# Optimization experiments

Hardware: AMD Instinct MI355X
Metric: run time of the kernel (lower is better)

The kernel has to match this reference:

```python
import jax, jax.numpy as jnp
import numpy as np

N = 27          # num_classes (nodes)
C = 512         # in_channels
B = 64          # batch
EPS = 1e-5


def _bn(x, gamma, beta):
    # BatchNorm1d over [b, channels, feat]: normalize over (batch, feat), training mode (batch stats, biased var)
    mean = jnp.mean(x, axis=(0, 2), keepdims=True)
    var = jnp.mean((x - mean) ** 2, axis=(0, 2), keepdims=True)
    return gamma[None, :, None] * (x - mean) * jax.lax.rsqrt(var + EPS) + beta[None, :, None]


def _layer(x, edge, WA, WB, WE, WU, WV, ge, be, gv, bv):
    # x: [b, n, c], edge: [b, n*n, c]; edge index e = i*n + j; end[e,i]=1, start[e,j]=1
    b = x.shape[0]
    res = x
    Vix = x @ WA.T                       # [b, n, c]  (gathered to edges via end)
    Vjx = x @ WB.T                       # [b, n, c]  (gathered to edges via start)
    e_lin = edge @ WE.T                  # [b, n*n, c]
    # einsum('ev,bvc->bec', end, Vix) == broadcast Vix over j; start gathers Vjx over i
    msg = (Vix[:, :, None, :] + Vjx[:, None, :, :]).reshape(b, N * N, C) + e_lin
    edge = edge + jax.nn.relu(_bn(msg, ge, be))
    # attention: sigmoid then softmax over j (dim 2 of [b, n, n, c])
    e = jax.nn.sigmoid(edge).reshape(b, N, N, C)
    e = jax.nn.softmax(e, axis=2).reshape(b, N * N, C)
    Ujx = x @ WV.T                       # [b, n, c], gathered via start -> broadcast over i
    Ujx_e = jnp.broadcast_to(Ujx[:, None, :, :], (b, N, N, C)).reshape(b, N * N, C)
    Uix = x @ WU.T
    # einsum('ve,bec->bvc', end.T, t) == sum over j of t[b, i*n+j]
    agg = (e * Ujx_e).reshape(b, N, N, C).sum(axis=2)
    x = Uix + agg / N
    x = jax.nn.relu(res + _bn(x, gv, bv))
    return x, edge


def setup_inputs() -> dict:
    key = jax.random.key(0)
    ks = jax.random.split(key, 12)
    scale = np.sqrt(2.0 / C)
    w = lambda k: (jax.random.normal(k, (C, C), dtype=jnp.float32) * scale)
    inp = {
        "x": jax.random.normal(ks[0], (B, N, C), dtype=jnp.float32),
        "edge": jax.random.normal(ks[1], (B, N * N, C), dtype=jnp.float32),
        "WU1": w(ks[2]), "WV1": w(ks[3]), "WA1": w(ks[4]), "WB1": w(ks[5]), "WE1": w(ks[6]),
        "WU2": w(ks[7]), "WV2": w(ks[8]), "WA2": w(ks[9]), "WB2": w(ks[10]), "WE2": w(ks[11]),
        "gv1": jnp.ones((N,), jnp.float32), "bv1": jnp.zeros((N,), jnp.float32),
        "ge1": jnp.ones((N * N,), jnp.float32), "be1": jnp.zeros((N * N,), jnp.float32),
        "gv2": jnp.ones((N,), jnp.float32), "bv2": jnp.zeros((N,), jnp.float32),
        "ge2": jnp.ones((N * N,), jnp.float32), "be2": jnp.zeros((N * N,), jnp.float32),
    }
    return inp


def reference(x, edge, WU1, WV1, WA1, WB1, WE1, WU2, WV2, WA2, WB2, WE2,
              gv1, bv1, ge1, be1, gv2, bv2, ge2, be2):
    x, edge = _layer(x, edge, WA1, WB1, WE1, WU1, WV1, ge1, be1, gv1, bv1)
    x, edge = _layer(x, edge, WA2, WB2, WE2, WU2, WV2, ge2, be2, gv2, bv2)
    return x, edge
```

## Files before the change

kernel.cpp:

```cpp
#include <hip/hip_runtime.h>

typedef unsigned short u16;
typedef unsigned int u32;
typedef __bf16 bf16x8 __attribute__((ext_vector_type(8)));
typedef float f32x4 __attribute__((ext_vector_type(4)));

#define DI __device__ __forceinline__

DI u16 f2bf(float f) {
  union { float f; u32 u; } v; v.f = f;
  return (u16)((v.u + 0x7fffu + ((v.u >> 16) & 1u)) >> 16);
}
DI float bf2f(u16 h) {
  union { u32 u; float f; } v; v.u = ((u32)h) << 16;
  return v.f;
}

DI void gload_lds16(const void* g, void* l) {
  __builtin_amdgcn_global_load_lds((const __attribute__((address_space(1))) u32*)g,
                                   (__attribute__((address_space(3))) u32*)l, 16, 0, 0);
}

constexpr float INV_M = 1.0f / 32768.0f;

__global__ void convw_k(const float* wa1, const float* wb1, const float* wu1, const float* wv1, const float* we1,
                        const float* wa2, const float* wb2, const float* wu2, const float* wv2, const float* we2,
                        u16* dst) {
  int idx = blockIdx.x * 256 + threadIdx.x;
  int m = idx >> 16;
  int i = (idx & 0xffff) << 2;
  const float* s;
  switch (m) {
    case 0: s = wa1; break; case 1: s = wb1; break; case 2: s = wu1; break;
    case 3: s = wv1; break; case 4: s = we1; break; case 5: s = wa2; break;
    case 6: s = wb2; break; case 7: s = wu2; break; case 8: s = wv2; break;
    default: s = we2; break;
  }
  float4 v = *(const float4*)(s + i);
  ushort4 o;
  o.x = f2bf(v.x); o.y = f2bf(v.y); o.z = f2bf(v.z); o.w = f2bf(v.w);
  *(ushort4*)(dst + ((size_t)m << 18) + i) = o;
}

template<int EPI, int ABF>
__global__ __launch_bounds__(256, 5) void gemm_k(
    const void* __restrict__ A_, const u16* __restrict__ W,
    float* __restrict__ outf, int ldout,
    u16* __restrict__ msg, const float* __restrict__ V4,
    float* __restrict__ esum, float* __restrict__ esq) {
  __shared__ __align__(16) u16 lA[64 * 64];
  __shared__ __align__(16) u16 lW[128 * 64];
  const int tid = threadIdx.x;
  const int lane = tid & 63, wid = tid >> 6;
  const int wm = wid >> 1, wn = wid & 1;
  const int q = lane >> 4, l15 = lane & 15;
  const int rb = blockIdx.y, cb = blockIdx.x;
  const int lrow8 = lane >> 3, lg = lane & 7;

  f32x4 acc[2][4];
#pragma unroll
  for (int a = 0; a < 2; a++)
#pragma unroll
    for (int b = 0; b < 4; b++) acc[a][b] = (f32x4){0.f, 0.f, 0.f, 0.f};

  for (int k0 = 0; k0 < 512; k0 += 64) {
    __syncthreads();
    if (ABF) {
#pragma unroll
      for (int it = 0; it < 2; it++) {
        int ch = wid * 2 + it;
        int row = ch * 8 + lrow8;
        const u16* src = (const u16*)A_ + (((size_t)(rb * 64 + row)) << 9) + k0 + ((lg ^ (row & 7)) << 3);
        gload_lds16(src, lA + ch * 512);
      }
    } else {
#pragma unroll
      for (int s = tid; s < 512; s += 256) {
        int row = s >> 3, g = s & 7;
        const float* src = (const float*)A_ + (((size_t)(rb * 64 + row)) << 9) + k0 + g * 8;
        float4 s0 = *(const float4*)src;
        float4 s1 = *(const float4*)(src + 4);
        uint4 p;
        p.x = f2bf(s0.x) | ((u32)f2bf(s0.y) << 16);
        p.y = f2bf(s0.z) | ((u32)f2bf(s0.w) << 16);
        p.z = f2bf(s1.x) | ((u32)f2bf(s1.y) << 16);
        p.w = f2bf(s1.z) | ((u32)f2bf(s1.w) << 16);
        *(uint4*)(lA + row * 64 + ((g ^ (row & 7)) << 3)) = p;
      }
    }
#pragma unroll
    for (int it = 0; it < 4; it++) {
      int ch = wid * 4 + it;
      int row = ch * 8 + lrow8;
      const u16* src = W + (((size_t)(cb * 128 + row)) << 9) + k0 + ((lg ^ (row & 7)) << 3);
      gload_lds16(src, lW + ch * 512);
    }
    __syncthreads();
#pragma unroll
    for (int ks = 0; ks < 2; ks++) {
      const int gk = ks * 4 + q;
      bf16x8 af[2], wf[4];
#pragma unroll
      for (int mt = 0; mt < 2; mt++) {
        int r = wm * 32 + mt * 16 + l15;
        af[mt] = *(const bf16x8*)(lA + r * 64 + ((gk ^ (r & 7)) << 3));
      }
#pragma unroll
      for (int nt = 0; nt < 4; nt++) {
        int r = wn * 64 + nt * 16 + l15;
        wf[nt] = *(const bf16x8*)(lW + r * 64 + ((gk ^ (r & 7)) << 3));
      }
#pragma unroll
      for (int mt = 0; mt < 2; mt++)
#pragma unroll
        for (int nt = 0; nt < 4; nt++)
          acc[mt][nt] = __builtin_amdgcn_mfma_f32_16x16x32_bf16(af[mt], wf[nt], acc[mt][nt], 0, 0, 0);
    }
  }

  if (EPI == 1) {
#pragma unroll
    for (int mt = 0; mt < 2; mt++) {
      int grow0 = rb * 64 + wm * 32 + mt * 16 + q * 4;
#pragma unroll
      for (int nt = 0; nt < 4; nt++) {
        int gcol = cb * 128 + wn * 64 + nt * 16 + l15;
#pragma unroll
        for (int r = 0; r < 4; r++)
          outf[(size_t)(grow0 + r) * ldout + gcol] = acc[mt][nt][r];
      }
    }
  } else {
    float ms[2][4], m2[2][4];
#pragma unroll
    for (int mt = 0; mt < 2; mt++) {
#pragma unroll
      for (int r = 0; r < 4; r++) {
        int grow = rb * 64 + wm * 32 + mt * 16 + q * 4 + r;
        int b = grow / 729;
        int e = grow - b * 729;
        int i = e / 27;
        int j = e - i * 27;
        const float* vix = V4 + (((size_t)(b * 27 + i)) << 11);
        const float* vjx = V4 + (((size_t)(b * 27 + j)) << 11) + 512;
        u16* mrow = msg + (((size_t)grow) << 9);
        float s1 = 0.f, s2 = 0.f;
#pragma unroll
        for (int nt = 0; nt < 4; nt++) {
          int c = cb * 128 + wn * 64 + nt * 16 + l15;
          float m = acc[mt][nt][r] + vix[c] + vjx[c];
          mrow[c] = f2bf(m);
          s1 += m;
          s2 += m * m;
        }
        ms[mt][r] = s1;
        m2[mt][r] = s2;
      }
    }
#pragma unroll
    for (int msk = 1; msk < 16; msk <<= 1) {
#pragma unroll
      for (int mt = 0; mt < 2; mt++)
#pragma unroll
        for (int r = 0; r < 4; r++) {
          ms[mt][r] += __shfl_xor(ms[mt][r], msk);
          m2[mt][r] += __shfl_xor(m2[mt][r], msk);
        }
    }
    __syncthreads();
    float* sm = (float*)lA;
    if (l15 == 0) {
#pragma unroll
      for (int mt = 0; mt < 2; mt++)
#pragma unroll
        for (int r = 0; r < 4; r++) {
          int rib = wm * 32 + mt * 16 + q * 4 + r;
          sm[wn * 64 + rib] = ms[mt][r];
          sm[128 + wn * 64 + rib] = m2[mt][r];
        }
    }
    __syncthreads();
    if (tid < 64) {
      int grow = rb * 64 + tid;
      int e = grow % 729;
      atomicAdd(&esum[e], sm[tid] + sm[64 + tid]);
      atomicAdd(&esq[e], sm[128 + tid] + sm[192 + tid]);
    }
  }
}

template<int INBF, int OUTBF>
__global__ __launch_bounds__(512) void edge_attn_k(
    const u16* msg, const void* ein_, void* eout_,
    const float* __restrict__ esum, const float* __restrict__ esq,
    const float* __restrict__ ge, const float* __restrict__ be,
    const float* __restrict__ V4,
    float* __restrict__ xnew, float* __restrict__ vsum, float* __restrict__ vsq) {
  const int bi = blockIdx.x;
  const int b = bi / 27, i = bi - b * 27;
  const int c = threadIdx.x;
  __shared__ float2 sab[27];
  if (c < 27) {
    int e = i * 27 + c;
    float mean = esum[e] * INV_M;
    float var = esq[e] * INV_M - mean * mean;
    float a = ge[e] * rsqrtf(var + 1e-5f);
    sab[c] = make_float2(a, be[e] - mean * a);
  }
  __syncthreads();
  const size_t ebase = (((size_t)(b * 729 + i * 27)) << 9) + c;
  const u16* einb = (const u16*)ein_;
  const float* einf = (const float*)ein_;
  u16* eoutb = (u16*)eout_;
  float* eoutf = (float*)eout_;
  float texp[27];
  float ssum = 0.f;
#pragma unroll
  for (int j = 0; j < 27; j++) {
    size_t idx = ebase + (((size_t)j) << 9);
    float2 ab = sab[j];
    float bn = fmaf(ab.x, bf2f(msg[idx]), ab.y);
    float ei = INBF ? bf2f(einb[idx]) : einf[idx];
    float eo = ei + fmaxf(bn, 0.f);
    if (OUTBF) eoutb[idx] = f2bf(eo); else eoutf[idx] = eo;
    float s = 1.f / (1.f + __expf(-eo));
    float t = __expf(s);
    ssum += t;
    texp[j] = t;
  }
  float accv = 0.f;
#pragma unroll
  for (int j = 0; j < 27; j++)
    accv = fmaf(texp[j], V4[(((size_t)(b * 27 + j)) << 11) + 1536 + c], accv);
  float xn = V4[(((size_t)(b * 27 + i)) << 11) + 1024 + c] + accv / (ssum * 27.f);
  xnew[(((size_t)bi) << 9) + c] = xn;
  float v = xn, v2 = xn * xn;
#pragma unroll
  for (int m = 32; m >= 1; m >>= 1) {
    v += __shfl_xor(v, m);
    v2 += __shfl_xor(v2, m);
  }
  __shared__ float red[16];
  int w = threadIdx.x >> 6, ln = threadIdx.x & 63;
  if (ln == 0) { red[w] = v; red[8 + w] = v2; }
  __syncthreads();
  if (threadIdx.x == 0) {
    float s1 = 0.f, s2 = 0.f;
#pragma unroll
    for (int k = 0; k < 8; k++) { s1 += red[k]; s2 += red[8 + k]; }
    atomicAdd(&vsum[i], s1);
    atomicAdd(&vsq[i], s2);
  }
}

__global__ void vert_bn_k(const float* __restrict__ xnew, const float* __restrict__ res,
                          const float* __restrict__ vsum, const float* __restrict__ vsq,
                          const float* __restrict__ g, const float* __restrict__ bt,
                          float* __restrict__ out) {
  int idx = blockIdx.x * 256 + threadIdx.x;
  int i = (idx >> 9) % 27;
  float mean = vsum[i] * INV_M;
  float var = vsq[i] * INV_M - mean * mean;
  float rs = rsqrtf(var + 1e-5f);
  float a = g[i] * rs;
  float bb = bt[i] - mean * a;
  out[idx] = fmaxf(res[idx] + fmaf(a, xnew[idx], bb), 0.f);
}

extern "C" void kernel_launch(void* const* d_in, const int* in_sizes, int n_in,
                              void* d_out, int out_size, void* d_ws, size_t ws_size,
                              hipStream_t stream) {
  const float* x    = (const float*)d_in[0];
  const float* edge = (const float*)d_in[1];
  const float* WU1 = (const float*)d_in[2];
  const float* WV1 = (const float*)d_in[3];
  const float* WA1 = (const float*)d_in[4];
  const float* WB1 = (const float*)d_in[5];
  const float* WE1 = (const float*)d_in[6];
  const float* WU2 = (const float*)d_in[7];
  const float* WV2 = (const float*)d_in[8];
  const float* WA2 = (const float*)d_in[9];
  const float* WB2 = (const float*)d_in[10];
  const float* WE2 = (const float*)d_in[11];
  const float* gv1 = (const float*)d_in[12];
  const float* bv1 = (const float*)d_in[13];
  const float* ge1 = (const float*)d_in[14];
  const float* be1 = (const float*)d_in[15];
  const float* gv2 = (const float*)d_in[16];
  const float* bv2 = (const float*)d_in[17];
  const float* ge2 = (const float*)d_in[18];
  const float* be2 = (const float*)d_in[19];

  char* ws = (char*)d_ws;
  u16*   wbf  = (u16*)(ws + 0);
  float* V4   = (float*)(ws + 5242880);
  u16*   M1   = (u16*)(ws + 19398656);
  u16*   M2   = (u16*)(ws + 67174400);
  float* xnew = (float*)(ws + 114950144);
  float* x1   = (float*)(ws + 118489088);
  float* st   = (float*)(ws + 122028032);
  float* es1 = st;         float* eq1 = st + 729;
  float* es2 = st + 1458;  float* eq2 = st + 2187;
  float* vs1 = st + 2916;  float* vq1 = st + 2943;
  float* vs2 = st + 2970;  float* vq2 = st + 2997;

  float* xout = (float*)d_out;
  float* eo   = (float*)d_out + 884736;

  hipMemsetAsync(st, 0, 3024 * sizeof(float), stream);
  convw_k<<<dim3(2560), dim3(256), 0, stream>>>(WA1, WB1, WU1, WV1, WE1, WA2, WB2, WU2, WV2, WE2, wbf);

  gemm_k<1, 0><<<dim3(16, 27), dim3(256), 0, stream>>>(x, wbf, V4, 2048, nullptr, nullptr, nullptr, nullptr);
  gemm_k<2, 0><<<dim3(4, 729), dim3(256), 0, stream>>>(edge, wbf + 4 * 262144, nullptr, 0, M1, V4, es1, eq1);
  edge_attn_k<0, 1><<<dim3(1728), dim3(512), 0, stream>>>(M1, edge, M1, es1, eq1, ge1, be1, V4, xnew, vs1, vq1);
  vert_bn_k<<<dim3(3456), dim3(256), 0, stream>>>(xnew, x, vs1, vq1, gv1, bv1, x1);

  gemm_k<1, 0><<<dim3(16, 27), dim3(256), 0, stream>>>(x1, wbf + 5 * 262144, V4, 2048, nullptr, nullptr, nullptr, nullptr);
  gemm_k<2, 1><<<dim3(4, 729), dim3(256), 0, stream>>>(M1, wbf + 9 * 262144, nullptr, 0, M2, V4, es2, eq2);
  edge_attn_k<1, 0><<<dim3(1728), dim3(512), 0, stream>>>(M2, M1, eo, es2, eq2, ge2, be2, V4, xnew, vs2, vq2);
  vert_bn_k<<<dim3(3456), dim3(256), 0, stream>>>(xnew, x1, vs2, vq2, gv2, bv2, xout);
}
```

Measured before the change: 480.2 us.

## Add XCD-aware block swizzle, narrower node GEMM tiles, and vectorized elementwise kernels

The edge GEMM now uses a 1D grid remapped so that the four column blocks of one row block land on the same XCD, which should improve L2 reuse of the A tile. Excess blocks exit early. The node GEMM uses 64-column tiles (NT=2) and twice as many blocks, for more parallelism on a small problem. The edge attention kernel now handles two channels per thread with packed 32-bit loads and stores in 256-thread blocks, and vert_bn uses float4. The costs are a few wasted blocks, higher register use from doubling the per-thread arrays, and a swizzle that relies on round-robin XCD dispatch.

```diff
diff --git a/kernel.cpp b/kernel.cpp
--- a/kernel.cpp
+++ b/kernel.cpp
@@ -42,26 +42,36 @@
   *(ushort4*)(dst + ((size_t)m << 18) + i) = o;
 }
 
-template<int EPI, int ABF>
+template<int EPI, int ABF, int SWZ, int NT>
 __global__ __launch_bounds__(256, 5) void gemm_k(
     const void* __restrict__ A_, const u16* __restrict__ W,
     float* __restrict__ outf, int ldout,
     u16* __restrict__ msg, const float* __restrict__ V4,
     float* __restrict__ esum, float* __restrict__ esq) {
   __shared__ __align__(16) u16 lA[64 * 64];
-  __shared__ __align__(16) u16 lW[128 * 64];
+  __shared__ __align__(16) u16 lW[32 * NT * 64];
   const int tid = threadIdx.x;
   const int lane = tid & 63, wid = tid >> 6;
   const int wm = wid >> 1, wn = wid & 1;
   const int q = lane >> 4, l15 = lane & 15;
-  const int rb = blockIdx.y, cb = blockIdx.x;
   const int lrow8 = lane >> 3, lg = lane & 7;
 
-  f32x4 acc[2][4];
+  int rb, cb;
+  if (SWZ) {
+    int l = blockIdx.x;
+    int xcd = l & 7, t = l >> 3;
+    cb = t & 3;
+    rb = ((t >> 2) << 3) | xcd;
+    if (rb >= 729) return;
+  } else {
+    rb = blockIdx.y; cb = blockIdx.x;
+  }
+
+  f32x4 acc[2][NT];
 #pragma unroll
   for (int a = 0; a < 2; a++)
 #pragma unroll
-    for (int b = 0; b < 4; b++) acc[a][b] = (f32x4){0.f, 0.f, 0.f, 0.f};
+    for (int b = 0; b < NT; b++) acc[a][b] = (f32x4){0.f, 0.f, 0.f, 0.f};
 
   for (int k0 = 0; k0 < 512; k0 += 64) {
     __syncthreads();
@@ -89,31 +99,31 @@
       }
     }
 #pragma unroll
-    for (int it = 0; it < 4; it++) {
-      int ch = wid * 4 + it;
+    for (int it = 0; it < NT; it++) {
+      int ch = wid * NT + it;
       int row = ch * 8 + lrow8;
-      const u16* src = W + (((size_t)(cb * 128 + row)) << 9) + k0 + ((lg ^ (row & 7)) << 3);
+      const u16* src = W + (((size_t)(cb * 32 * NT + row)) << 9) + k0 + ((lg ^ (row & 7)) << 3);
       gload_lds16(src, lW + ch * 512);
     }
     __syncthreads();
 #pragma unroll
     for (int ks = 0; ks < 2; ks++) {
       const int gk = ks * 4 + q;
-      bf16x8 af[2], wf[4];
+      bf16x8 af[2], wf[NT];
 #pragma unroll
       for (int mt = 0; mt < 2; mt++) {
         int r = wm * 32 + mt * 16 + l15;
         af[mt] = *(const bf16x8*)(lA + r * 64 + ((gk ^ (r & 7)) << 3));
       }
 #pragma unroll
-      for (int nt = 0; nt < 4; nt++) {
-        int r = wn * 64 + nt * 16 + l15;
+      for (int nt = 0; nt < NT; nt++) {
+        int r = wn * 16 * NT + nt * 16 + l15;
         wf[nt] = *(const bf16x8*)(lW + r * 64 + ((gk ^ (r & 7)) << 3));
       }
 #pragma unroll
       for (int mt = 0; mt < 2; mt++)
 #pragma unroll
-        for (int nt = 0; nt < 4; nt++)
+        for (int nt = 0; nt < NT; nt++)
           acc[mt][nt] = __builtin_amdgcn_mfma_f32_16x16x32_bf16(af[mt], wf[nt], acc[mt][nt], 0, 0, 0);
     }
   }
@@ -123,8 +133,8 @@
     for (int mt = 0; mt < 2; mt++) {
       int grow0 = rb * 64 + wm * 32 + mt * 16 + q * 4;
 #pragma unroll
-      for (int nt = 0; nt < 4; nt++) {
-        int gcol = cb * 128 + wn * 64 + nt * 16 + l15;
+      for (int nt = 0; nt < NT; nt++) {
+        int gcol = cb * 32 * NT + wn * 16 * NT + nt * 16 + l15;
 #pragma unroll
         for (int r = 0; r < 4; r++)
           outf[(size_t)(grow0 + r) * ldout + gcol] = acc[mt][nt][r];
@@ -146,8 +156,8 @@
         u16* mrow = msg + (((size_t)grow) << 9);
         float s1 = 0.f, s2 = 0.f;
 #pragma unroll
-        for (int nt = 0; nt < 4; nt++) {
-          int c = cb * 128 + wn * 64 + nt * 16 + l15;
+        for (int nt = 0; nt < NT; nt++) {
+          int c = cb * 32 * NT + wn * 16 * NT + nt * 16 + l15;
           float m = acc[mt][nt][r] + vix[c] + vjx[c];
           mrow[c] = f2bf(m);
           s1 += m;
@@ -190,81 +200,103 @@
 }
 
 template<int INBF, int OUTBF>
-__global__ __launch_bounds__(512) void edge_attn_k(
-    const u16* msg, const void* ein_, void* eout_,
+__global__ __launch_bounds__(256) void edge_attn_k(
+    const u16* __restrict__ msg, const void* __restrict__ ein_, void* __restrict__ eout_,
     const float* __restrict__ esum, const float* __restrict__ esq,
     const float* __restrict__ ge, const float* __restrict__ be,
     const float* __restrict__ V4,
     float* __restrict__ xnew, float* __restrict__ vsum, float* __restrict__ vsq) {
   const int bi = blockIdx.x;
   const int b = bi / 27, i = bi - b * 27;
-  const int c = threadIdx.x;
+  const int t = threadIdx.x;
   __shared__ float2 sab[27];
-  if (c < 27) {
-    int e = i * 27 + c;
+  if (t < 27) {
+    int e = i * 27 + t;
     float mean = esum[e] * INV_M;
     float var = esq[e] * INV_M - mean * mean;
     float a = ge[e] * rsqrtf(var + 1e-5f);
-    sab[c] = make_float2(a, be[e] - mean * a);
+    sab[t] = make_float2(a, be[e] - mean * a);
   }
   __syncthreads();
-  const size_t ebase = (((size_t)(b * 729 + i * 27)) << 9) + c;
+  const size_t ebase = (((size_t)(b * 729 + i * 27)) << 9) + 2 * t;
   const u16* einb = (const u16*)ein_;
   const float* einf = (const float*)ein_;
   u16* eoutb = (u16*)eout_;
   float* eoutf = (float*)eout_;
-  float texp[27];
-  float ssum = 0.f;
+  float t0[27], t1[27];
+  float ss0 = 0.f, ss1 = 0.f;
 #pragma unroll
   for (int j = 0; j < 27; j++) {
     size_t idx = ebase + (((size_t)j) << 9);
     float2 ab = sab[j];
-    float bn = fmaf(ab.x, bf2f(msg[idx]), ab.y);
-    float ei = INBF ? bf2f(einb[idx]) : einf[idx];
-    float eo = ei + fmaxf(bn, 0.f);
-    if (OUTBF) eoutb[idx] = f2bf(eo); else eoutf[idx] = eo;
-    float s = 1.f / (1.f + __expf(-eo));
-    float t = __expf(s);
-    ssum += t;
-    texp[j] = t;
-  }
-  float accv = 0.f;
-#pragma unroll
-  for (int j = 0; j < 27; j++)
-    accv = fmaf(texp[j], V4[(((size_t)(b * 27 + j)) << 11) + 1536 + c], accv);
-  float xn = V4[(((size_t)(b * 27 + i)) << 11) + 1024 + c] + accv / (ssum * 27.f);
-  xnew[(((size_t)bi) << 9) + c] = xn;
-  float v = xn, v2 = xn * xn;
+    u32 mp = *(const u32*)(msg + idx);
+    float2 ei;
+    if (INBF) {
+      u32 ep = *(const u32*)(einb + idx);
+      ei = make_float2(bf2f((u16)ep), bf2f((u16)(ep >> 16)));
+    } else {
+      ei = *(const float2*)(einf + idx);
+    }
+    float e0 = ei.x + fmaxf(fmaf(ab.x, bf2f((u16)mp), ab.y), 0.f);
+    float e1 = ei.y + fmaxf(fmaf(ab.x, bf2f((u16)(mp >> 16)), ab.y), 0.f);
+    if (OUTBF) {
+      *(u32*)(eoutb + idx) = (u32)f2bf(e0) | ((u32)f2bf(e1) << 16);
+    } else {
+      *(float2*)(eoutf + idx) = make_float2(e0, e1);
+    }
+    float x0 = __expf(1.f / (1.f + __expf(-e0)));
+    float x1 = __expf(1.f / (1.f + __expf(-e1)));
+    ss0 += x0; ss1 += x1;
+    t0[j] = x0; t1[j] = x1;
+  }
+  float a0 = 0.f, a1 = 0.f;
+#pragma unroll
+  for (int j = 0; j < 27; j++) {
+    float2 uj = *(const float2*)(V4 + (((size_t)(b * 27 + j)) << 11) + 1536 + 2 * t);
+    a0 = fmaf(t0[j], uj.x, a0);
+    a1 = fmaf(t1[j], uj.y, a1);
+  }
+  float2 ui = *(const float2*)(V4 + (((size_t)(b * 27 + i)) << 11) + 1024 + 2 * t);
+  float xn0 = ui.x + a0 / (ss0 * 27.f);
+  float xn1 = ui.y + a1 / (ss1 * 27.f);
+  *(float2*)(xnew + (((size_t)bi) << 9) + 2 * t) = make_float2(xn0, xn1);
+  float v = xn0 + xn1, v2 = xn0 * xn0 + xn1 * xn1;
 #pragma unroll
   for (int m = 32; m >= 1; m >>= 1) {
     v += __shfl_xor(v, m);
     v2 += __shfl_xor(v2, m);
   }
-  __shared__ float red[16];
-  int w = threadIdx.x >> 6, ln = threadIdx.x & 63;
-  if (ln == 0) { red[w] = v; red[8 + w] = v2; }
+  __shared__ float red[8];
+  int w = t >> 6, ln = t & 63;
+  if (ln == 0) { red[w] = v; red[4 + w] = v2; }
   __syncthreads();
-  if (threadIdx.x == 0) {
+  if (t == 0) {
     float s1 = 0.f, s2 = 0.f;
 #pragma unroll
-    for (int k = 0; k < 8; k++) { s1 += red[k]; s2 += red[8 + k]; }
+    for (int k = 0; k < 4; k++) { s1 += red[k]; s2 += red[4 + k]; }
     atomicAdd(&vsum[i], s1);
     atomicAdd(&vsq[i], s2);
   }
 }
 
-__global__ void vert_bn_k(const float* __restrict__ xnew, const float* __restrict__ res,
+__global__ void vert_bn_k(const float4* __restrict__ xnew, const float4* __restrict__ res,
                           const float* __restrict__ vsum, const float* __restrict__ vsq,
                           const float* __restrict__ g, const float* __restrict__ bt,
-                          float* __restrict__ out) {
+                          float4* __restrict__ out) {
   int idx = blockIdx.x * 256 + threadIdx.x;
-  int i = (idx >> 9) % 27;
+  int i = (idx >> 7) % 27;
   float mean = vsum[i] * INV_M;
   float var = vsq[i] * INV_M - mean * mean;
-  float rs = rsqrtf(var + 1e-5f);
-  float a = g[i] * rs;
+  float a = g[i] * rsqrtf(var + 1e-5f);
   float bb = bt[i] - mean * a;
-  out[idx] = fmaxf(res[idx] + fmaf(a, xnew[idx], bb), 0.f);
+  float4 xv = xnew[idx];
+  float4 rv = res[idx];
+  float4 o;
+  o.x = fmaxf(rv.x + fmaf(a, xv.x, bb), 0.f);
+  o.y = fmaxf(rv.y + fmaf(a, xv.y, bb), 0.f);
+  o.z = fmaxf(rv.z + fmaf(a, xv.z, bb), 0.f);
+  o.w = fmaxf(rv.w + fmaf(a, xv.w, bb), 0.f);
+  out[idx] = o;
 }
 
 extern "C" void kernel_launch(void* const* d_in, const int* in_sizes, int n_in,
@@ -310,13 +342,13 @@
   hipMemsetAsync(st, 0, 3024 * sizeof(float), stream);
   convw_k<<<dim3(2560), dim3(256), 0, stream>>>(WA1, WB1, WU1, WV1, WE1, WA2, WB2, WU2, WV2, WE2, wbf);
 
-  gemm_k<1, 0><<<dim3(16, 27), dim3(256), 0, stream>>>(x, wbf, V4, 2048, nullptr, nullptr, nullptr, nullptr);
-  gemm_k<2, 0><<<dim3(4, 729), dim3(256), 0, stream>>>(edge, wbf + 4 * 262144, nullptr, 0, M1, V4, es1, eq1);
-  edge_attn_k<0, 1><<<dim3(1728), dim3(512), 0, stream>>>(M1, edge, M1, es1, eq1, ge1, be1, V4, xnew, vs1, vq1);
-  vert_bn_k<<<dim3(3456), dim3(256), 0, stream>>>(xnew, x, vs1, vq1, gv1, bv1, x1);
-
-  gemm_k<1, 0><<<dim3(16, 27), dim3(256), 0, stream>>>(x1, wbf + 5 * 262144, V4, 2048, nullptr, nullptr, nullptr, nullptr);
-  gemm_k<2, 1><<<dim3(4, 729), dim3(256), 0, stream>>>(M1, wbf + 9 * 262144, nullptr, 0, M2, V4, es2, eq2);
-  edge_attn_k<1, 0><<<dim3(1728), dim3(512), 0, stream>>>(M2, M1, eo, es2, eq2, ge2, be2, V4, xnew, vs2, vq2);
-  vert_bn_k<<<dim3(3456), dim3(256), 0, stream>>>(xnew, x1, vs2, vq2, gv2, bv2, xout);
-}
+  gemm_k<1, 0, 0, 2><<<dim3(32, 27), dim3(256), 0, stream>>>(x, wbf, V4, 2048, nullptr, nullptr, nullptr, nullptr);
+  gemm_k<2, 0, 1, 4><<<dim3(2944), dim3(256), 0, stream>>>(edge, wbf + 4 * 262144, nullptr, 0, M1, V4, es1, eq1);
+  edge_attn_k<0, 1><<<dim3(1728), dim3(256), 0, stream>>>(M1, edge, M1, es1, eq1, ge1, be1, V4, xnew, vs1, vq1);
+  vert_bn_k<<<dim3(864), dim3(256), 0, stream>>>((const float4*)xnew, (const float4*)x, vs1, vq1, gv1, bv1, (float4*)x1);
+
+  gemm_k<1, 0, 0, 2><<<dim3(32, 27), dim3(256), 0, stream>>>(x1, wbf + 5 * 262144, V4, 2048, nullptr, nullptr, nullptr, nullptr);
+  gemm_k<2, 1, 1, 4><<<dim3(2944), dim3(256), 0, stream>>>(M1, wbf + 9 * 262144, nullptr, 0, M2, V4, es2, eq2);
+  edge_attn_k<1, 0><<<dim3(1728), dim3(256), 0, stream>>>(M2, M1, eo, es2, eq2, ge2, be2, V4, xnew, vs2, vq2);
+  vert_bn_k<<<dim3(864), dim3(256), 0, stream>>>((const float4*)xnew, (const float4*)x1, vs2, vq2, gv2, bv2, (float4*)xout);
+}
```

After: 442.0 us. -8.0%, faster.
